# Kernel tuning notes

Measured on AMD Instinct MI355X. Metric: run time of the kernel, lower is better.

Reference implementation:

```python
import jax, jax.numpy as jnp
import numpy as np

T = 8192          # sequence length
E = 1024          # embedding_dim
H = 1024          # hidden_dim
HD = H // 2       # per-direction hidden
K = 34            # tagset size
START, STOP = 32, 33
NEG = -10000.0


def setup_inputs() -> dict:
    key = jax.random.key(0)
    ks = jax.random.split(key, 16)
    s = 1.0 / np.sqrt(HD)  # torch LSTM/Linear init scale
    u = lambda k, shp, sc: jax.random.uniform(k, shp, jnp.float32, -sc, sc)
    inp = {
        "sentence": jax.random.normal(ks[0], (T, E), jnp.float32),
        "h0": jax.random.normal(ks[1], (2, HD), jnp.float32),
        "c0": jax.random.normal(ks[2], (2, HD), jnp.float32),
        "w_ih_f": u(ks[3], (4 * HD, E), s),
        "w_hh_f": u(ks[4], (4 * HD, HD), s),
        "b_ih_f": u(ks[5], (4 * HD,), s),
        "b_hh_f": u(ks[6], (4 * HD,), s),
        "w_ih_b": u(ks[7], (4 * HD, E), s),
        "w_hh_b": u(ks[8], (4 * HD, HD), s),
        "b_ih_b": u(ks[9], (4 * HD,), s),
        "b_hh_b": u(ks[10], (4 * HD,), s),
        "w_out": u(ks[11], (K, H), 1.0 / np.sqrt(H)),
        "b_out": u(ks[12], (K,), 1.0 / np.sqrt(H)),
    }
    trans = jax.random.normal(ks[13], (K, K), jnp.float32)
    trans = trans.at[START, :].set(NEG).at[:, STOP].set(NEG)
    inp["transitions"] = trans
    return inp


def _lstm_dir(x_proj, h0, c0, w_hh, reverse):
    # x_proj: [T, 4*HD] precomputed input projection (+ both biases)
    def step(carry, xp):
        h, c = carry
        g = xp + h @ w_hh.T
        i, f, gg, o = jnp.split(g, 4)
        i, f, o = jax.nn.sigmoid(i), jax.nn.sigmoid(f), jax.nn.sigmoid(o)
        c = f * c + i * jnp.tanh(gg)
        h = o * jnp.tanh(c)
        return (h, c), h
    _, hs = jax.lax.scan(step, (h0, c0), x_proj, reverse=reverse)
    return hs  # [T, HD]


def reference(sentence, h0, c0, w_ih_f, w_hh_f, b_ih_f, b_hh_f,
              w_ih_b, w_hh_b, b_ih_b, b_hh_b, w_out, b_out, transitions):
    # BiLSTM encoder (dropout is identity at inference)
    xp_f = sentence @ w_ih_f.T + (b_ih_f + b_hh_f)
    xp_b = sentence @ w_ih_b.T + (b_ih_b + b_hh_b)
    hs_f = _lstm_dir(xp_f, h0[0], c0[0], w_hh_f, reverse=False)
    hs_b = _lstm_dir(xp_b, h0[1], c0[1], w_hh_b, reverse=True)
    lstm_out = jnp.concatenate([hs_f, hs_b], axis=-1)        # [T, H]
    feats = lstm_out @ w_out.T + b_out                        # [T, K]

    # Viterbi decode: scores[next, prev] = fv[prev] + transitions[next, prev]
    fv0 = jnp.full((K,), NEG, jnp.float32).at[START].set(0.0)

    def vit_step(fv, feat):
        scores = fv[None, :] + transitions                    # [K, K]
        bp = jnp.argmax(scores, axis=1)                       # best prev per next
        fv_new = jnp.max(scores, axis=1) + feat
        return fv_new, bp

    fv, bps = jax.lax.scan(vit_step, fv0, feats)              # bps: [T, K]
    terminal = fv + transitions[STOP]
    best_last = jnp.argmax(terminal)
    path_score = terminal[best_last]

    def back_step(tag, bp_t):
        return bp_t[tag], tag

    _, best_path = jax.lax.scan(back_step, best_last, bps, reverse=True)  # [T]
    return path_score, best_path, sentence
```

## Files before the change

kernel.cpp:

```cpp
#include <hip/hip_runtime.h>
#include <hip/hip_bf16.h>

typedef float v4f __attribute__((ext_vector_type(4)));
typedef int   v4i __attribute__((ext_vector_type(4)));

#define T_LEN 8192
#define E_DIM 1024
#define HD    512
#define G4    2048
#define K_TAGS 34

#define XP_OFF      0ull
#define HS_OFF      134217728ull
#define FEATS_OFF   167772160ull
#define BP_OFF      168886272ull
#define BEST_OFF    169165824ull

#define BM 128
#define BN 128
#define BKK 16

__global__ __launch_bounds__(256) void xp_gemm(
    const float* __restrict__ A, const float* __restrict__ Wf, const float* __restrict__ Wb,
    const float* __restrict__ bihf, const float* __restrict__ bhhf,
    const float* __restrict__ bihb, const float* __restrict__ bhhb,
    float* __restrict__ xp)
{
  __shared__ __align__(16) float a_lds[BKK][BM + 4];
  __shared__ __align__(16) float b_lds[BKK][BN + 4];
  const int dir = blockIdx.z;
  const float* W   = dir ? Wb : Wf;
  const float* bih = dir ? bihb : bihf;
  const float* bhh = dir ? bhhb : bhhf;
  const int tid = threadIdx.x;
  const int srow = tid >> 1, sh = (tid & 1) * 8;
  const int tx = tid & 15, ty = tid >> 4;
  const size_t arow = (size_t)(blockIdx.x * BM + srow) * E_DIM;
  const size_t brow = (size_t)(blockIdx.y * BN + srow) * E_DIM;
  float acc[8][8];
  #pragma unroll
  for (int i = 0; i < 8; ++i)
    #pragma unroll
    for (int j = 0; j < 8; ++j) acc[i][j] = 0.f;

  for (int k0 = 0; k0 < E_DIM; k0 += BKK) {
    v4f a0 = *(const v4f*)(A + arow + k0 + sh);
    v4f a1 = *(const v4f*)(A + arow + k0 + sh + 4);
    v4f b0 = *(const v4f*)(W + brow + k0 + sh);
    v4f b1 = *(const v4f*)(W + brow + k0 + sh + 4);
    __syncthreads();
    #pragma unroll
    for (int j = 0; j < 4; ++j) {
      a_lds[sh + j][srow]     = a0[j];
      a_lds[sh + 4 + j][srow] = a1[j];
      b_lds[sh + j][srow]     = b0[j];
      b_lds[sh + 4 + j][srow] = b1[j];
    }
    __syncthreads();
    #pragma unroll
    for (int kk = 0; kk < BKK; ++kk) {
      v4f av0 = *(const v4f*)&a_lds[kk][ty * 8];
      v4f av1 = *(const v4f*)&a_lds[kk][ty * 8 + 4];
      v4f bv0 = *(const v4f*)&b_lds[kk][tx * 4];
      v4f bv1 = *(const v4f*)&b_lds[kk][64 + tx * 4];
      float av[8] = {av0[0],av0[1],av0[2],av0[3],av1[0],av1[1],av1[2],av1[3]};
      float bv[8] = {bv0[0],bv0[1],bv0[2],bv0[3],bv1[0],bv1[1],bv1[2],bv1[3]};
      #pragma unroll
      for (int i = 0; i < 8; ++i)
        #pragma unroll
        for (int j = 0; j < 8; ++j) acc[i][j] = fmaf(av[i], bv[j], acc[i][j]);
    }
  }
  const int gm  = blockIdx.x * BM + ty * 8;
  const int gnl = blockIdx.y * BN + tx * 4;
  const int gnh = gnl + 64;
  float bias[8];
  #pragma unroll
  for (int j = 0; j < 4; ++j) bias[j]     = bih[gnl + j] + bhh[gnl + j];
  #pragma unroll
  for (int j = 0; j < 4; ++j) bias[4 + j] = bih[gnh + j] + bhh[gnh + j];
  float* outp = xp + ((size_t)dir * T_LEN) * G4;
  #pragma unroll
  for (int i = 0; i < 8; ++i) {
    v4f o0 = {acc[i][0]+bias[0], acc[i][1]+bias[1], acc[i][2]+bias[2], acc[i][3]+bias[3]};
    v4f o1 = {acc[i][4]+bias[4], acc[i][5]+bias[5], acc[i][6]+bias[6], acc[i][7]+bias[7]};
    *(v4f*)(outp + (size_t)(gm + i) * G4 + gnl) = o0;
    *(v4f*)(outp + (size_t)(gm + i) * G4 + gnh) = o1;
  }
}

__device__ __forceinline__ float row16_sum(float x) {
  x += __int_as_float(__builtin_amdgcn_update_dpp(0, __float_as_int(x), 0x111, 0xf, 0xf, true));
  x += __int_as_float(__builtin_amdgcn_update_dpp(0, __float_as_int(x), 0x112, 0xf, 0xf, true));
  x += __int_as_float(__builtin_amdgcn_update_dpp(0, __float_as_int(x), 0x114, 0xf, 0xf, true));
  x += __int_as_float(__builtin_amdgcn_update_dpp(0, __float_as_int(x), 0x118, 0xf, 0xf, true));
  return x;
}

__device__ __forceinline__ float sigmoidf_(float x) { return 1.f / (1.f + expf(-x)); }

__global__ __launch_bounds__(1024) void lstm_kernel(
    const float* __restrict__ h0, const float* __restrict__ c0,
    const float* __restrict__ whhf, const float* __restrict__ whhb,
    const float* __restrict__ xp, float* __restrict__ hs)
{
  const int b = blockIdx.x;
  const int dir = b >> 5, bb = b & 31;
  const int tid = threadIdx.x;
  const int w = tid >> 6, L = tid & 63;
  const float* whh = dir ? whhb : whhf;
  const float* xpd = xp + (size_t)dir * T_LEN * G4;
  float* hsd = hs + (size_t)dir * T_LEN * HD;
  __shared__ __align__(16) float red2[16][4][4];
  __shared__ __align__(16) float hl[HD];
  __shared__ float xpl[2][64];
  __shared__ float gl[4][16];

  float wreg[4][8];
  #pragma unroll
  for (int j = 0; j < 4; ++j) {
    int r = 4 * w + j;
    int grow = (r >> 4) * HD + bb * 16 + (r & 15);
    const float* p = whh + (size_t)grow * HD + 8 * L;
    v4f q0 = *(const v4f*)p;
    v4f q1 = *(const v4f*)(p + 4);
    #pragma unroll
    for (int kk = 0; kk < 4; ++kk) { wreg[j][kk] = q0[kk]; wreg[j][4 + kk] = q1[kk]; }
  }
  float cst = (tid < 16) ? c0[dir * HD + bb * 16 + tid] : 0.f;
  if (tid >= 64 && tid < 128) {
    int r = tid - 64;
    int col = (r >> 4) * HD + bb * 16 + (r & 15);
    int t0 = dir ? (T_LEN - 1) : 0;
    xpl[0][r] = xpd[(size_t)t0 * G4 + col];
  }
  __syncthreads();

  for (int s = 0; s < T_LEN; ++s) {
    const int t = dir ? (T_LEN - 1 - s) : s;

    if (w == 0) {
      if (s == 0) {
        const float* hp = h0 + dir * HD + 8 * L;
        v4f a = *(const v4f*)hp;
        v4f bq = *(const v4f*)(hp + 4);
        *(v4f*)&hl[8 * L]     = a;
        *(v4f*)&hl[8 * L + 4] = bq;
      } else {
        const int tp = dir ? (t + 1) : (t - 1);
        const float* hp = hsd + (size_t)tp * HD + 8 * L;
        v4i ia, ib;
        do {
          asm volatile("global_load_dwordx4 %0, %2, off sc0 sc1\n"
                       "global_load_dwordx4 %1, %2, off offset:16 sc0 sc1\n"
                       "s_waitcnt vmcnt(0)"
                       : "=&v"(ia), "=&v"(ib) : "v"(hp) : "memory");
        } while (((ia[0] == -1) | (ia[1] == -1) | (ia[2] == -1) | (ia[3] == -1) |
                  (ib[0] == -1) | (ib[1] == -1) | (ib[2] == -1) | (ib[3] == -1)) != 0);
        v4f fa, fb;
        #pragma unroll
        for (int kk = 0; kk < 4; ++kk) { fa[kk] = __int_as_float(ia[kk]); fb[kk] = __int_as_float(ib[kk]); }
        *(v4f*)&hl[8 * L]     = fa;
        *(v4f*)&hl[8 * L + 4] = fb;
      }
    }
    __syncthreads();

    v4f h0v = *(const v4f*)&hl[8 * L];
    v4f h1v = *(const v4f*)&hl[8 * L + 4];
    float hr[8] = {h0v[0], h0v[1], h0v[2], h0v[3], h1v[0], h1v[1], h1v[2], h1v[3]};
    float a4[4];
    #pragma unroll
    for (int j = 0; j < 4; ++j) {
      float a = 0.f;
      #pragma unroll
      for (int kk = 0; kk < 8; ++kk) a = fmaf(wreg[j][kk], hr[kk], a);
      a4[j] = row16_sum(a);
    }
    if ((L & 15) == 15) {
      int q = L >> 4;
      v4f rv = {a4[0], a4[1], a4[2], a4[3]};
      *(v4f*)&red2[w][q][0] = rv;
    }
    __syncthreads();

    if (tid < 64) {
      const int u = tid & 15, g = tid >> 4;
      const int r = g * 16 + u;
      const int ww = r >> 2, j = r & 3;
      const float sum = red2[ww][0][j] + red2[ww][1][j] + red2[ww][2][j] + red2[ww][3][j]
                      + xpl[s & 1][r];
      const float gv = (g == 2) ? tanhf(sum) : sigmoidf_(sum);
      gl[g][u] = gv;
      asm volatile("s_waitcnt lgkmcnt(0)" ::: "memory");
      if (tid < 16) {
        const float ig = gl[0][u];
        const float fg = gl[1][u];
        const float gg = gl[2][u];
        const float og = gl[3][u];
        cst = fg * cst + ig * gg;
        const float hval = og * tanhf(cst);
        float* hp = hsd + (size_t)t * HD + bb * 16 + u;
        asm volatile("global_store_dword %0, %1, off sc0 sc1" :: "v"(hp), "v"(hval) : "memory");
      }
    } else if (tid >= 64 && tid < 128 && s + 1 < T_LEN) {
      const int r = tid - 64;
      const int col = (r >> 4) * HD + bb * 16 + (r & 15);
      const int tn = dir ? (t - 1) : (t + 1);
      xpl[(s + 1) & 1][r] = xpd[(size_t)tn * G4 + col];
    }
  }
}

__global__ __launch_bounds__(256) void feats_kernel(
    const float* __restrict__ hs, const float* __restrict__ wout,
    const float* __restrict__ bout, float* __restrict__ feats)
{
  __shared__ __align__(16) float xs[32][132];
  __shared__ __align__(16) float wl[34][132];
  const int tid = threadIdx.x;
  const int t0 = blockIdx.x * 32;
  const int m = tid & 31, ng = tid >> 5;
  float acc[5] = {0.f, 0.f, 0.f, 0.f, 0.f};
  for (int cc = 0; cc < 8; ++cc) {
    const int d = cc >> 2;
    const int c0 = (cc & 3) * 128;
    const float* hsrc = hs + (size_t)d * T_LEN * HD;
    const int wcol = d * HD + c0;
    __syncthreads();
    {
      const int row = tid >> 3, seg = tid & 7;
      const float* src = hsrc + (size_t)(t0 + row) * HD + c0 + seg * 16;
      #pragma unroll
      for (int i = 0; i < 4; ++i) {
        v4f v = *(const v4f*)(src + i * 4);
        *(v4f*)&xs[row][seg * 16 + i * 4] = v;
      }
    }
    for (int i = tid; i < 34 * 32; i += 256) {
      const int r = i >> 5, q = i & 31;
      v4f v = *(const v4f*)(wout + (size_t)r * E_DIM + wcol + q * 4);
      *(v4f*)&wl[r][q * 4] = v;
    }
    __syncthreads();
    for (int kq = 0; kq < 32; ++kq) {
      v4f xv = *(const v4f*)&xs[m][kq * 4];
      #pragma unroll
      for (int sl = 0; sl < 5; ++sl) {
        const int n = ng + sl * 8;
        if (n < K_TAGS) {
          v4f wv = *(const v4f*)&wl[n][kq * 4];
          acc[sl] = fmaf(xv[0], wv[0], acc[sl]);
          acc[sl] = fmaf(xv[1], wv[1], acc[sl]);
          acc[sl] = fmaf(xv[2], wv[2], acc[sl]);
          acc[sl] = fmaf(xv[3], wv[3], acc[sl]);
        }
      }
    }
  }
  #pragma unroll
  for (int sl = 0; sl < 5; ++sl) {
    const int n = ng + sl * 8;
    if (n < K_TAGS) feats[(size_t)(t0 + m) * K_TAGS + n] = acc[sl] + bout[n];
  }
}

__global__ __launch_bounds__(64) void viterbi_kernel(
    const float* __restrict__ feats, const float* __restrict__ trans,
    float* __restrict__ d_out, int* __restrict__ bestlast, unsigned char* __restrict__ bp)
{
  const int L = threadIdx.x;
  const int n = (L < K_TAGS) ? L : 0;
  const bool act = (L < K_TAGS);
  float tr[K_TAGS];
  #pragma unroll
  for (int p = 0; p < K_TAGS; ++p) tr[p] = trans[n * K_TAGS + p];
  const float tstop = trans[33 * K_TAGS + n];
  __shared__ float fvs[K_TAGS];
  if (act) fvs[n] = (n == 32) ? 0.f : -10000.f;
  asm volatile("s_waitcnt lgkmcnt(0)" ::: "memory");
  __builtin_amdgcn_sched_barrier(0);

  float feat_next = feats[n];
  float fvreg = 0.f;
  for (int t = 0; t < T_LEN; ++t) {
    const float feat = feat_next;
    if (t + 1 < T_LEN) feat_next = feats[(size_t)(t + 1) * K_TAGS + n];
    float val[K_TAGS];
    int   idx[K_TAGS];
    #pragma unroll
    for (int p = 0; p < K_TAGS; ++p) { val[p] = fvs[p] + tr[p]; idx[p] = p; }
    #pragma unroll
    for (int st = 1; st < K_TAGS; st <<= 1) {
      #pragma unroll
      for (int i = 0; i + st < K_TAGS; i += 2 * st) {
        if (val[i + st] > val[i]) { val[i] = val[i + st]; idx[i] = idx[i + st]; }
      }
    }
    fvreg = val[0] + feat;
    if (act) {
      bp[(size_t)t * K_TAGS + n] = (unsigned char)idx[0];
      fvs[n] = fvreg;
    }
    asm volatile("s_waitcnt lgkmcnt(0)" ::: "memory");
    __builtin_amdgcn_sched_barrier(0);
  }
  if (act) fvs[n] = fvreg + tstop;
  asm volatile("s_waitcnt lgkmcnt(0)" ::: "memory");
  __builtin_amdgcn_sched_barrier(0);
  if (L == 0) {
    float best = -3.4e38f; int bi = 0;
    for (int k = 0; k < K_TAGS; ++k) {
      const float v = fvs[k];
      if (v > best) { best = v; bi = k; }
    }
    d_out[0] = best;
    *bestlast = bi;
  }
}

__global__ __launch_bounds__(1024) void backtrace_kernel(
    const unsigned char* __restrict__ bp, const int* __restrict__ bestlast,
    float* __restrict__ d_out)
{
  __shared__ unsigned char exitl[128 * K_TAGS];
  __shared__ unsigned char entl[128];
  const int tid = threadIdx.x;
  for (int W = tid; W < 128 * K_TAGS; W += 1024) {
    const int c = W / K_TAGS;
    int tg = W % K_TAGS;
    for (int t = c * 64 + 63; t >= c * 64; --t) tg = bp[(size_t)t * K_TAGS + tg];
    exitl[W] = (unsigned char)tg;
  }
  __syncthreads();
  if (tid == 0) {
    int tag = *bestlast;
    entl[127] = (unsigned char)tag;
    for (int c = 127; c >= 1; --c) {
      tag = exitl[c * K_TAGS + tag];
      entl[c - 1] = (unsigned char)tag;
    }
  }
  __syncthreads();
  if (tid < 128) {
    const int c = tid;
    int tg = entl[c];
    for (int t = c * 64 + 63; t >= c * 64; --t) {
      d_out[1 + t] = (float)tg;
      tg = bp[(size_t)t * K_TAGS + tg];
    }
  }
}

extern "C" void kernel_launch(void* const* d_in, const int* in_sizes, int n_in,
                              void* d_out, int out_size, void* d_ws, size_t ws_size,
                              hipStream_t stream)
{
  const float* sent = (const float*)d_in[0];
  const float* h0   = (const float*)d_in[1];
  const float* c0   = (const float*)d_in[2];
  const float* wihf = (const float*)d_in[3];
  const float* whhf = (const float*)d_in[4];
  const float* bihf = (const float*)d_in[5];
  const float* bhhf = (const float*)d_in[6];
  const float* wihb = (const float*)d_in[7];
  const float* whhb = (const float*)d_in[8];
  const float* bihb = (const float*)d_in[9];
  const float* bhhb = (const float*)d_in[10];
  const float* wout = (const float*)d_in[11];
  const float* bout = (const float*)d_in[12];
  const float* trans = (const float*)d_in[13];

  float* out = (float*)d_out;
  char* ws = (char*)d_ws;
  float* xp    = (float*)(ws + XP_OFF);
  float* hs    = (float*)(ws + HS_OFF);
  float* feats = (float*)(ws + FEATS_OFF);
  unsigned char* bp = (unsigned char*)(ws + BP_OFF);
  int* bestlast = (int*)(ws + BEST_OFF);

  hipMemsetAsync(hs, 0xFF, (size_t)2 * T_LEN * HD * sizeof(float), stream);

  hipMemcpyAsync(out + 1 + T_LEN, sent, (size_t)T_LEN * E_DIM * sizeof(float),
                 hipMemcpyDeviceToDevice, stream);

  dim3 g1(T_LEN / BM, G4 / BN, 2);
  xp_gemm<<<g1, 256, 0, stream>>>(sent, wihf, wihb, bihf, bhhf, bihb, bhhb, xp);

  lstm_kernel<<<64, 1024, 0, stream>>>(h0, c0, whhf, whhb, xp, hs);

  feats_kernel<<<T_LEN / 32, 256, 0, stream>>>(hs, wout, bout, feats);

  viterbi_kernel<<<1, 64, 0, stream>>>(feats, trans, out, bestlast, bp);

  backtrace_kernel<<<1, 1024, 0, stream>>>(bp, bestlast, out);
}
```

Measured before the change: 19.80 ms.

## Restructure LSTM step sync: LDS flag handoff, wave-local reduction, redundant gate math

Result: slower. 22.25 ms (+12.4%).

```diff
diff --git a/kernel.cpp b/kernel.cpp
--- a/kernel.cpp
+++ b/kernel.cpp
@@ -111,103 +111,113 @@
   const float* whh = dir ? whhb : whhf;
   const float* xpd = xp + (size_t)dir * T_LEN * G4;
   float* hsd = hs + (size_t)dir * T_LEN * HD;
-  __shared__ __align__(16) float red2[16][4][4];
-  __shared__ __align__(16) float hl[HD];
-  __shared__ float xpl[2][64];
-  __shared__ float gl[4][16];
+
+  __shared__ __align__(16) float hl[2][HD];
+  __shared__ float gt[2][4][16];
+  volatile __shared__ int hrdy[2];
 
   float wreg[4][8];
   #pragma unroll
-  for (int j = 0; j < 4; ++j) {
-    int r = 4 * w + j;
-    int grow = (r >> 4) * HD + bb * 16 + (r & 15);
+  for (int g = 0; g < 4; ++g) {
+    const int grow = g * HD + bb * 16 + w;
     const float* p = whh + (size_t)grow * HD + 8 * L;
     v4f q0 = *(const v4f*)p;
     v4f q1 = *(const v4f*)(p + 4);
     #pragma unroll
-    for (int kk = 0; kk < 4; ++kk) { wreg[j][kk] = q0[kk]; wreg[j][4 + kk] = q1[kk]; }
-  }
-  float cst = (tid < 16) ? c0[dir * HD + bb * 16 + tid] : 0.f;
-  if (tid >= 64 && tid < 128) {
-    int r = tid - 64;
-    int col = (r >> 4) * HD + bb * 16 + (r & 15);
-    int t0 = dir ? (T_LEN - 1) : 0;
-    xpl[0][r] = xpd[(size_t)t0 * G4 + col];
-  }
+    for (int kk = 0; kk < 4; ++kk) { wreg[g][kk] = q0[kk]; wreg[g][4 + kk] = q1[kk]; }
+  }
+  float cst = (L < 16) ? c0[dir * HD + bb * 16 + L] : 0.f;
+  const int xcol = (L >> 4) * HD + bb * 16 + (L & 15);
+  float xpc = xpd[(size_t)(dir ? (T_LEN - 1) : 0) * G4 + xcol];
+
+  if (tid == 0) { hrdy[0] = 0; hrdy[1] = 0; }
   __syncthreads();
 
   for (int s = 0; s < T_LEN; ++s) {
     const int t = dir ? (T_LEN - 1 - s) : s;
-
-    if (w == 0) {
-      if (s == 0) {
-        const float* hp = h0 + dir * HD + 8 * L;
-        v4f a = *(const v4f*)hp;
-        v4f bq = *(const v4f*)(hp + 4);
-        *(v4f*)&hl[8 * L]     = a;
-        *(v4f*)&hl[8 * L + 4] = bq;
-      } else {
-        const int tp = dir ? (t + 1) : (t - 1);
-        const float* hp = hsd + (size_t)tp * HD + 8 * L;
-        v4i ia, ib;
-        do {
-          asm volatile("global_load_dwordx4 %0, %2, off sc0 sc1\n"
-                       "global_load_dwordx4 %1, %2, off offset:16 sc0 sc1\n"
-                       "s_waitcnt vmcnt(0)"
-                       : "=&v"(ia), "=&v"(ib) : "v"(hp) : "memory");
-        } while (((ia[0] == -1) | (ia[1] == -1) | (ia[2] == -1) | (ia[3] == -1) |
-                  (ib[0] == -1) | (ib[1] == -1) | (ib[2] == -1) | (ib[3] == -1)) != 0);
-        v4f fa, fb;
-        #pragma unroll
-        for (int kk = 0; kk < 4; ++kk) { fa[kk] = __int_as_float(ia[kk]); fb[kk] = __int_as_float(ib[kk]); }
-        *(v4f*)&hl[8 * L]     = fa;
-        *(v4f*)&hl[8 * L + 4] = fb;
+    const int sl = s & 1;
+
+    float hr[8];
+    if (s == 0) {
+      const float* hp = h0 + dir * HD + 8 * L;
+      v4f a = *(const v4f*)hp;
+      v4f bq = *(const v4f*)(hp + 4);
+      #pragma unroll
+      for (int kk = 0; kk < 4; ++kk) { hr[kk] = a[kk]; hr[4 + kk] = bq[kk]; }
+    } else if (w >= 14) {
+      const int tp = dir ? (t + 1) : (t - 1);
+      const float* hp = hsd + (size_t)tp * HD + 8 * L;
+      v4i ia, ib;
+      do {
+        asm volatile("global_load_dwordx4 %0, %2, off sc0 sc1\n"
+                     "global_load_dwordx4 %1, %2, off offset:16 sc0 sc1\n"
+                     "s_waitcnt vmcnt(0)"
+                     : "=&v"(ia), "=&v"(ib) : "v"(hp) : "memory");
+      } while (((ia[0] == -1) | (ia[1] == -1) | (ia[2] == -1) | (ia[3] == -1) |
+                (ib[0] == -1) | (ib[1] == -1) | (ib[2] == -1) | (ib[3] == -1)) != 0);
+      v4f fa, fb;
+      #pragma unroll
+      for (int kk = 0; kk < 4; ++kk) {
+        fa[kk] = __int_as_float(ia[kk]);
+        fb[kk] = __int_as_float(ib[kk]);
+        hr[kk] = fa[kk]; hr[4 + kk] = fb[kk];
       }
+      *(v4f*)&hl[sl][8 * L]     = fa;
+      *(v4f*)&hl[sl][8 * L + 4] = fb;
+      asm volatile("s_waitcnt lgkmcnt(0)" ::: "memory");
+      if (L == 0) atomicAdd((int*)&hrdy[sl], 1);
+    } else {
+      while (hrdy[sl] < 2) { }
+      asm volatile("s_waitcnt lgkmcnt(0)" ::: "memory");
+      __builtin_amdgcn_sched_barrier(0);
+      v4f a = *(const v4f*)&hl[sl][8 * L];
+      v4f bq = *(const v4f*)&hl[sl][8 * L + 4];
+      #pragma unroll
+      for (int kk = 0; kk < 4; ++kk) { hr[kk] = a[kk]; hr[4 + kk] = bq[kk]; }
+    }
+
+    float tot[4];
+    #pragma unroll
+    for (int g = 0; g < 4; ++g) {
+      float a = 0.f;
+      #pragma unroll
+      for (int kk = 0; kk < 8; ++kk) a = fmaf(wreg[g][kk], hr[kk], a);
+      const float rs = row16_sum(a);
+      const float s0 = __shfl(rs, 15);
+      const float s1 = __shfl(rs, 31);
+      const float s2 = __shfl(rs, 47);
+      const float s3 = __shfl(rs, 63);
+      tot[g] = ((s0 + s1) + s2) + s3;
+    }
+    {
+      const float lo = (L & 2) ? tot[2] : tot[0];
+      const float hi = (L & 2) ? tot[3] : tot[1];
+      const float myv = (L & 1) ? hi : lo;
+      if (L < 4) gt[sl][L][w] = myv;
     }
     __syncthreads();
-
-    v4f h0v = *(const v4f*)&hl[8 * L];
-    v4f h1v = *(const v4f*)&hl[8 * L + 4];
-    float hr[8] = {h0v[0], h0v[1], h0v[2], h0v[3], h1v[0], h1v[1], h1v[2], h1v[3]};
-    float a4[4];
-    #pragma unroll
-    for (int j = 0; j < 4; ++j) {
-      float a = 0.f;
-      #pragma unroll
-      for (int kk = 0; kk < 8; ++kk) a = fmaf(wreg[j][kk], hr[kk], a);
-      a4[j] = row16_sum(a);
-    }
-    if ((L & 15) == 15) {
-      int q = L >> 4;
-      v4f rv = {a4[0], a4[1], a4[2], a4[3]};
-      *(v4f*)&red2[w][q][0] = rv;
-    }
-    __syncthreads();
-
-    if (tid < 64) {
-      const int u = tid & 15, g = tid >> 4;
-      const int r = g * 16 + u;
-      const int ww = r >> 2, j = r & 3;
-      const float sum = red2[ww][0][j] + red2[ww][1][j] + red2[ww][2][j] + red2[ww][3][j]
-                      + xpl[s & 1][r];
+    if (tid == 0) hrdy[sl] = 0;
+
+    {
+      const int g = L >> 4, u = L & 15;
+      const float sum = gt[sl][g][u] + xpc;
       const float gv = (g == 2) ? tanhf(sum) : sigmoidf_(sum);
-      gl[g][u] = gv;
-      asm volatile("s_waitcnt lgkmcnt(0)" ::: "memory");
-      if (tid < 16) {
-        const float ig = gl[0][u];
-        const float fg = gl[1][u];
-        const float gg = gl[2][u];
-        const float og = gl[3][u];
+      const float ig = __shfl(gv, u);
+      const float fg = __shfl(gv, u + 16);
+      const float gg = __shfl(gv, u + 32);
+      const float og = __shfl(gv, u + 48);
+      if (L < 16) {
         cst = fg * cst + ig * gg;
         const float hval = og * tanhf(cst);
-        float* hp = hsd + (size_t)t * HD + bb * 16 + u;
-        asm volatile("global_store_dword %0, %1, off sc0 sc1" :: "v"(hp), "v"(hval) : "memory");
+        if (w == 0) {
+          float* hp = hsd + (size_t)t * HD + bb * 16 + L;
+          asm volatile("global_store_dword %0, %1, off sc0 sc1" :: "v"(hp), "v"(hval) : "memory");
+        }
       }
-    } else if (tid >= 64 && tid < 128 && s + 1 < T_LEN) {
-      const int r = tid - 64;
-      const int col = (r >> 4) * HD + bb * 16 + (r & 15);
+    }
+    if (s + 1 < T_LEN) {
       const int tn = dir ? (t - 1) : (t + 1);
-      xpl[(s + 1) & 1][r] = xpd[(size_t)tn * G4 + col];
+      xpc = xpd[(size_t)tn * G4 + xcol];
     }
   }
 }
```
